# Performance work log

Measured on AMD Instinct MI355X. Metric: run time of the kernel, lower is better.

Reference implementation:

```python
import jax, jax.numpy as jnp
import numpy as np

B, N, D = 2, 2048, 1024
H = 16
HD = D // H
SCALE = HD ** -0.5


def setup_inputs() -> dict:
    key = jax.random.key(0)
    k1, k2, kw, kb = jax.random.split(key, 4)
    x1 = jax.random.normal(k1, (B, N, D), dtype=jnp.float32)
    x2 = jax.random.normal(k2, (B, N, D), dtype=jnp.float32)
    # fused qkv linear: torch nn.Linear(dim, 3*dim): W [3D, D], b [3D]
    bound = 1.0 / np.sqrt(D)
    qkv_w = jax.random.uniform(kw, (3 * D, D), minval=-bound, maxval=bound, dtype=jnp.float32)
    qkv_b = jax.random.uniform(kb, (3 * D,), minval=-bound, maxval=bound, dtype=jnp.float32)
    return {"x1": x1, "x2": x2, "qkv_w": qkv_w, "qkv_b": qkv_b}


def reference(x1, x2, qkv_w, qkv_b):
    # qkv projections (only q from x1 and k,v from x2 are used by the module)
    q1 = (jnp.einsum('bnd,ed->bne', x1, qkv_w[:D]) + qkv_b[:D])
    k2 = (jnp.einsum('bnd,ed->bne', x2, qkv_w[D:2 * D]) + qkv_b[D:2 * D])
    v2 = (jnp.einsum('bnd,ed->bne', x2, qkv_w[2 * D:]) + qkv_b[2 * D:])
    # [B, H, N, HD]
    q1 = q1.reshape(B, N, H, HD).transpose(0, 2, 1, 3)
    k2 = k2.reshape(B, N, H, HD).transpose(0, 2, 1, 3)
    v2 = v2.reshape(B, N, H, HD).transpose(0, 2, 1, 3)
    # explicit QK^T -> softmax -> AV (materializes [B,H,N,N] like the original)
    scores = jnp.einsum('bhqd,bhkd->bhqk', q1, k2) * SCALE
    attn = jax.nn.softmax(scores, axis=-1)
    out = jnp.einsum('bhqk,bhkd->bhqd', attn, v2)
    # [B, N, D]; note original module skips out_proj (never applied in forward)
    return out.transpose(0, 2, 1, 3).reshape(B, N, D)
```

## Files before the change

kernel.cpp:

```cpp
#include <hip/hip_runtime.h>
#include <cstdint>
#include <cstddef>

#define B_   2
#define N_   2048
#define D_   1024
#define H_   16
#define HD_  64
#define QSCALE_ 0.18033688011112042f

typedef unsigned short u16;
typedef unsigned int   u32;
typedef __attribute__((ext_vector_type(8))) short short8;
typedef __attribute__((ext_vector_type(4))) float f32x4;
typedef __attribute__((ext_vector_type(4))) float fl4;
typedef __attribute__((ext_vector_type(4))) unsigned short us4;

__device__ __forceinline__ u16 f2bf(float f) {
  u32 u = __builtin_bit_cast(u32, f);
  u += 0x7fffu + ((u >> 16) & 1u);
  return (u16)(u >> 16);
}

__device__ __forceinline__ void gload16(const void* g, void* l) {
  typedef __attribute__((address_space(1))) unsigned int gu32;
  typedef __attribute__((address_space(3))) unsigned int lu32;
  __builtin_amdgcn_global_load_lds((gu32*)g, (lu32*)l, 16, 0, 0);
}

__global__ void convert_kernel(const fl4* __restrict__ x1, const fl4* __restrict__ x2,
                               const fl4* __restrict__ w,
                               us4* __restrict__ o1, us4* __restrict__ o2,
                               us4* __restrict__ ow) {
  const int NX = (B_ * N_ * D_) / 4;
  const int NW = (3 * D_ * D_) / 4;
  int stride = gridDim.x * blockDim.x;
  for (int i = blockIdx.x * blockDim.x + threadIdx.x; i < NX; i += stride) {
    fl4 a = x1[i];
    us4 r; r.x = f2bf(a.x); r.y = f2bf(a.y); r.z = f2bf(a.z); r.w = f2bf(a.w);
    o1[i] = r;
    fl4 b = x2[i];
    us4 s; s.x = f2bf(b.x); s.y = f2bf(b.y); s.z = f2bf(b.z); s.w = f2bf(b.w);
    o2[i] = s;
    if (i < NW) {
      fl4 c = w[i];
      us4 t; t.x = f2bf(c.x); t.y = f2bf(c.y); t.z = f2bf(c.z); t.w = f2bf(c.w);
      ow[i] = t;
    }
  }
}

__global__ __launch_bounds__(256) void qkv_gemm(
    const u16* __restrict__ x1b, const u16* __restrict__ x2b,
    const u16* __restrict__ wb, const float* __restrict__ bias,
    u16* __restrict__ Qb, u16* __restrict__ Kb, u16* __restrict__ Vtb) {
  const int z = blockIdx.z;
  const u16* X = (z == 0) ? x1b : x2b;
  const u16* W = wb + (size_t)z * D_ * D_;
  const float* bz = bias + z * D_;
  const int m0 = blockIdx.y * 128;
  const int e0 = blockIdx.x * 128;
  const int tid = threadIdx.x;
  const int lane = tid & 63;
  const int w = tid >> 6;
  const int wr = w >> 1, wc = w & 1;
  const int col = lane & 15, quad = lane >> 4;

  __shared__ __align__(16) u16 As[128 * 32];
  __shared__ __align__(16) u16 Bs[128 * 32];

  f32x4 acc[4][4] = {};

  int off0 = w * 2048 + lane * 16;
  int row0 = off0 >> 6;
  int ke0  = (off0 & 63) >> 1;
  int off1 = off0 + 1024;
  int row1 = off1 >> 6;
  int ke1  = (off1 & 63) >> 1;

  const u16* gA0 = X + (size_t)(m0 + row0) * D_ + ke0;
  const u16* gA1 = X + (size_t)(m0 + row1) * D_ + ke1;
  const u16* gB0 = W + (size_t)(e0 + row0) * D_ + ke0;
  const u16* gB1 = W + (size_t)(e0 + row1) * D_ + ke1;
  u16* lA0 = &As[w * 1024];
  u16* lA1 = &As[w * 1024 + 512];
  u16* lB0 = &Bs[w * 1024];
  u16* lB1 = &Bs[w * 1024 + 512];

  for (int k0 = 0; k0 < D_; k0 += 32) {
    __syncthreads();
    gload16(gA0 + k0, lA0);
    gload16(gA1 + k0, lA1);
    gload16(gB0 + k0, lB0);
    gload16(gB1 + k0, lB1);
    __syncthreads();

    short8 a[4], b[4];
#pragma unroll
    for (int i = 0; i < 4; ++i)
      a[i] = *(const short8*)&As[(wr * 64 + i * 16 + col) * 32 + quad * 8];
#pragma unroll
    for (int j = 0; j < 4; ++j)
      b[j] = *(const short8*)&Bs[(wc * 64 + j * 16 + col) * 32 + quad * 8];
#pragma unroll
    for (int i = 0; i < 4; ++i)
#pragma unroll
      for (int j = 0; j < 4; ++j)
        acc[i][j] = __builtin_amdgcn_mfma_f32_16x16x32_bf16(a[i], b[j], acc[i][j], 0, 0, 0);
  }

#pragma unroll
  for (int j = 0; j < 4; ++j) {
    int eg = e0 + wc * 64 + j * 16 + col;
    float bj = bz[eg];
    int h = eg >> 6, d = eg & 63;
#pragma unroll
    for (int i = 0; i < 4; ++i) {
#pragma unroll
      for (int r = 0; r < 4; ++r) {
        int m = m0 + wr * 64 + i * 16 + quad * 4 + r;
        int bb = m >> 11, n = m & (N_ - 1);
        float v = acc[i][j][r] + bj;
        if (z == 0) v *= QSCALE_;
        u16 o = f2bf(v);
        if (z == 0)      Qb [(((size_t)bb * H_ + h) * N_ + n) * HD_ + d] = o;
        else if (z == 1) Kb [(((size_t)bb * H_ + h) * N_ + n) * HD_ + d] = o;
        else             Vtb[(((size_t)bb * H_ + h) * HD_ + d) * N_ + n] = o;
      }
    }
  }
}

__global__ __launch_bounds__(256) void attn_kernel(
    const u16* __restrict__ Qb, const u16* __restrict__ Kb,
    const u16* __restrict__ Vtb, float* __restrict__ out) {
  const int bh = blockIdx.y;
  const int bb = bh >> 4, h = bh & 15;
  const int q0 = blockIdx.x * 64;
  const int tid = threadIdx.x;
  const int lane = tid & 63;
  const int w = tid >> 6;
  const int col = lane & 15, quad = lane >> 4;

  const u16* __restrict__ Q  = Qb  + ((size_t)bh << 17);
  const u16* __restrict__ K  = Kb  + ((size_t)bh << 17);
  const u16* __restrict__ Vt = Vtb + ((size_t)bh << 17);

  __shared__ __align__(16) u16 Ks[64 * 72];
  __shared__ __align__(16) u16 Vs[64 * 72];
  __shared__ __align__(16) u16 P[4][16 * 72];
  u16* Pw = P[w];

  const int qrow = q0 + w * 16 + col;
  short8 qa0 = *(const short8*)&Q[qrow * HD_ + quad * 8];
  short8 qa1 = *(const short8*)&Q[qrow * HD_ + 32 + quad * 8];

  const int srow = tid >> 3;
  const int sseg = (tid & 7) * 8;
  const u16* gK0 = &K[srow * HD_ + sseg];
  const u16* gK1 = &K[(srow + 32) * HD_ + sseg];
  const u16* gV0 = &Vt[srow * N_ + sseg];
  const u16* gV1 = &Vt[(srow + 32) * N_ + sseg];
  u16* lK0 = &Ks[srow * 72 + sseg];
  u16* lK1 = &Ks[(srow + 32) * 72 + sseg];
  u16* lV0 = &Vs[srow * 72 + sseg];
  u16* lV1 = &Vs[(srow + 32) * 72 + sseg];

  f32x4 accO[4] = {};
  float lsum[4] = {0.f, 0.f, 0.f, 0.f};

  short8 kA = *(const short8*)(gK0);
  short8 kB = *(const short8*)(gK1);
  short8 vA = *(const short8*)(gV0);
  short8 vB = *(const short8*)(gV1);

  for (int k0 = 0; k0 < N_; k0 += 64) {
    __syncthreads();
    *(short8*)lK0 = kA;
    *(short8*)lK1 = kB;
    *(short8*)lV0 = vA;
    *(short8*)lV1 = vB;
    if (k0 + 64 < N_) {
      kA = *(const short8*)(gK0 + (k0 + 64) * HD_);
      kB = *(const short8*)(gK1 + (k0 + 64) * HD_);
      vA = *(const short8*)(gV0 + (k0 + 64));
      vB = *(const short8*)(gV1 + (k0 + 64));
    }
    __syncthreads();

    f32x4 s[4] = {};
#pragma unroll
    for (int jn = 0; jn < 4; ++jn) {
      short8 kb0 = *(const short8*)&Ks[(jn * 16 + col) * 72 + quad * 8];
      short8 kb1 = *(const short8*)&Ks[(jn * 16 + col) * 72 + 32 + quad * 8];
      s[jn] = __builtin_amdgcn_mfma_f32_16x16x32_bf16(qa0, kb0, s[jn], 0, 0, 0);
      s[jn] = __builtin_amdgcn_mfma_f32_16x16x32_bf16(qa1, kb1, s[jn], 0, 0, 0);
    }

#pragma unroll
    for (int jn = 0; jn < 4; ++jn)
#pragma unroll
      for (int r = 0; r < 4; ++r) {
        float e = exp2f(s[jn][r]);
        lsum[r] += e;
        Pw[(quad * 4 + r) * 72 + jn * 16 + col] =
            (u16)(__builtin_bit_cast(u32, e) >> 16);
      }
    __asm__ volatile("" ::: "memory");
    short8 pa0 = *(const short8*)&Pw[col * 72 + quad * 8];
    short8 pa1 = *(const short8*)&Pw[col * 72 + 32 + quad * 8];
    __asm__ volatile("" ::: "memory");

#pragma unroll
    for (int jd = 0; jd < 4; ++jd) {
      short8 vb0 = *(const short8*)&Vs[(jd * 16 + col) * 72 + quad * 8];
      short8 vb1 = *(const short8*)&Vs[(jd * 16 + col) * 72 + 32 + quad * 8];
      accO[jd] = __builtin_amdgcn_mfma_f32_16x16x32_bf16(pa0, vb0, accO[jd], 0, 0, 0);
      accO[jd] = __builtin_amdgcn_mfma_f32_16x16x32_bf16(pa1, vb1, accO[jd], 0, 0, 0);
    }
  }

#pragma unroll
  for (int r = 0; r < 4; ++r) {
    float v = lsum[r];
    v += __shfl_xor(v, 1);
    v += __shfl_xor(v, 2);
    v += __shfl_xor(v, 4);
    v += __shfl_xor(v, 8);
    lsum[r] = 1.0f / v;
  }

#pragma unroll
  for (int jd = 0; jd < 4; ++jd)
#pragma unroll
    for (int r = 0; r < 4; ++r) {
      int n = q0 + w * 16 + quad * 4 + r;
      int e = h * HD_ + jd * 16 + col;
      out[((size_t)bb * N_ + n) * D_ + e] = accO[jd][r] * lsum[r];
    }
}

extern "C" void kernel_launch(void* const* d_in, const int* in_sizes, int n_in,
                              void* d_out, int out_size, void* d_ws, size_t ws_size,
                              hipStream_t stream) {
  const float* x1 = (const float*)d_in[0];
  const float* x2 = (const float*)d_in[1];
  const float* qw = (const float*)d_in[2];
  const float* qb = (const float*)d_in[3];
  float* out = (float*)d_out;

  u16* ws   = (u16*)d_ws;
  u16* x1b  = ws;
  u16* x2b  = ws + 4194304;
  u16* wb   = ws + 8388608;
  u16* Qbf  = ws + 11534336;
  u16* Kbf  = ws + 15728640;
  u16* Vtb  = ws + 19922944;
  if (ws_size < (size_t)24117248 * 2) return;

  convert_kernel<<<dim3(1024), dim3(256), 0, stream>>>(
      (const fl4*)x1, (const fl4*)x2, (const fl4*)qw,
      (us4*)x1b, (us4*)x2b, (us4*)wb);

  qkv_gemm<<<dim3(8, 32, 3), dim3(256), 0, stream>>>(
      x1b, x2b, wb, qb, Qbf, Kbf, Vtb);

  attn_kernel<<<dim3(32, 32), dim3(256), 0, stream>>>(Qbf, Kbf, Vtb, out);
}
```

Baseline: 205.0 us.

## Double-buffer K/V tiles in attention with XOR-swizzled LDS and one barrier

```diff
diff --git a/kernel.cpp b/kernel.cpp
--- a/kernel.cpp
+++ b/kernel.cpp
@@ -15,6 +15,12 @@
 typedef __attribute__((ext_vector_type(4))) float f32x4;
 typedef __attribute__((ext_vector_type(4))) float fl4;
 typedef __attribute__((ext_vector_type(4))) unsigned short us4;
+
+#if __has_builtin(__builtin_amdgcn_exp2f)
+#define EXP2F(x) __builtin_amdgcn_exp2f(x)
+#else
+#define EXP2F(x) exp2f(x)
+#endif
 
 __device__ __forceinline__ u16 f2bf(float f) {
   u32 u = __builtin_bit_cast(u32, f);
@@ -131,7 +137,7 @@
   }
 }
 
-__global__ __launch_bounds__(256) void attn_kernel(
+__global__ __launch_bounds__(256, 4) void attn_kernel(
     const u16* __restrict__ Qb, const u16* __restrict__ Kb,
     const u16* __restrict__ Vtb, float* __restrict__ out) {
   const int bh = blockIdx.y;
@@ -146,77 +152,98 @@
   const u16* __restrict__ K  = Kb  + ((size_t)bh << 17);
   const u16* __restrict__ Vt = Vtb + ((size_t)bh << 17);
 
-  __shared__ __align__(16) u16 Ks[64 * 72];
-  __shared__ __align__(16) u16 Vs[64 * 72];
-  __shared__ __align__(16) u16 P[4][16 * 72];
+  __shared__ __align__(16) u16 Ks[2][64 * 64];
+  __shared__ __align__(16) u16 Vs[2][64 * 64];
+  __shared__ __align__(16) u16 P[4][16 * 64];
   u16* Pw = P[w];
 
   const int qrow = q0 + w * 16 + col;
   short8 qa0 = *(const short8*)&Q[qrow * HD_ + quad * 8];
   short8 qa1 = *(const short8*)&Q[qrow * HD_ + 32 + quad * 8];
 
+  const int g0  = (quad ^ (col & 7)) * 8;
+  const int g4  = g0 ^ 32;
+  const int pg0 = (quad ^ ((col >> 1) & 7)) * 8;
+  const int pg4 = pg0 ^ 32;
+  const int c3 = col >> 3, c7 = col & 7;
+  const int h2 = quad * 2;
+
   const int srow = tid >> 3;
-  const int sseg = (tid & 7) * 8;
-  const u16* gK0 = &K[srow * HD_ + sseg];
-  const u16* gK1 = &K[(srow + 32) * HD_ + sseg];
-  const u16* gV0 = &Vt[srow * N_ + sseg];
-  const u16* gV1 = &Vt[(srow + 32) * N_ + sseg];
-  u16* lK0 = &Ks[srow * 72 + sseg];
-  u16* lK1 = &Ks[(srow + 32) * 72 + sseg];
-  u16* lV0 = &Vs[srow * 72 + sseg];
-  u16* lV1 = &Vs[(srow + 32) * 72 + sseg];
+  const int sg   = tid & 7;
+  const int lw0 = srow * 64 + ((sg ^ (srow & 7)) * 8);
+  const int lw1 = lw0 + 2048;
+  const u16* gK = K + tid * 8;
+  const u16* gV = Vt + srow * N_ + sg * 8;
 
   f32x4 accO[4] = {};
   float lsum[4] = {0.f, 0.f, 0.f, 0.f};
 
-  short8 kA = *(const short8*)(gK0);
-  short8 kB = *(const short8*)(gK1);
-  short8 vA = *(const short8*)(gV0);
-  short8 vB = *(const short8*)(gV1);
-
-  for (int k0 = 0; k0 < N_; k0 += 64) {
+  short8 kA = *(const short8*)(gK);
+  short8 kB = *(const short8*)(gK + 2048);
+  short8 vA = *(const short8*)(gV);
+  short8 vB = *(const short8*)(gV + 32 * N_);
+  *(short8*)&Ks[0][lw0] = kA;
+  *(short8*)&Ks[0][lw1] = kB;
+  *(short8*)&Vs[0][lw0] = vA;
+  *(short8*)&Vs[0][lw1] = vB;
+
+  for (int t = 0; t < N_ / 64; ++t) {
     __syncthreads();
-    *(short8*)lK0 = kA;
-    *(short8*)lK1 = kB;
-    *(short8*)lV0 = vA;
-    *(short8*)lV1 = vB;
-    if (k0 + 64 < N_) {
-      kA = *(const short8*)(gK0 + (k0 + 64) * HD_);
-      kB = *(const short8*)(gK1 + (k0 + 64) * HD_);
-      vA = *(const short8*)(gV0 + (k0 + 64));
-      vB = *(const short8*)(gV1 + (k0 + 64));
-    }
-    __syncthreads();
+    const int cur = t & 1;
+    if (t < N_ / 64 - 1) {
+      const int k0n = (t + 1) * 64;
+      kA = *(const short8*)(gK + k0n * 64);
+      kB = *(const short8*)(gK + k0n * 64 + 2048);
+      vA = *(const short8*)(gV + k0n);
+      vB = *(const short8*)(gV + k0n + 32 * N_);
+    }
+    const u16* Kc = Ks[cur];
+    const u16* Vc = Vs[cur];
 
     f32x4 s[4] = {};
+    __builtin_amdgcn_s_setprio(1);
 #pragma unroll
     for (int jn = 0; jn < 4; ++jn) {
-      short8 kb0 = *(const short8*)&Ks[(jn * 16 + col) * 72 + quad * 8];
-      short8 kb1 = *(const short8*)&Ks[(jn * 16 + col) * 72 + 32 + quad * 8];
+      const int rb = (jn * 16 + col) * 64;
+      short8 kb0 = *(const short8*)&Kc[rb + g0];
+      short8 kb1 = *(const short8*)&Kc[rb + g4];
       s[jn] = __builtin_amdgcn_mfma_f32_16x16x32_bf16(qa0, kb0, s[jn], 0, 0, 0);
       s[jn] = __builtin_amdgcn_mfma_f32_16x16x32_bf16(qa1, kb1, s[jn], 0, 0, 0);
     }
+    __builtin_amdgcn_s_setprio(0);
 
 #pragma unroll
     for (int jn = 0; jn < 4; ++jn)
 #pragma unroll
       for (int r = 0; r < 4; ++r) {
-        float e = exp2f(s[jn][r]);
+        float e = EXP2F(s[jn][r]);
         lsum[r] += e;
-        Pw[(quad * 4 + r) * 72 + jn * 16 + col] =
+        Pw[(quad * 4 + r) * 64 + (((2 * jn + c3) ^ (h2 + (r >> 1))) * 8) + c7] =
             (u16)(__builtin_bit_cast(u32, e) >> 16);
       }
     __asm__ volatile("" ::: "memory");
-    short8 pa0 = *(const short8*)&Pw[col * 72 + quad * 8];
-    short8 pa1 = *(const short8*)&Pw[col * 72 + 32 + quad * 8];
+    short8 pa0 = *(const short8*)&Pw[col * 64 + pg0];
+    short8 pa1 = *(const short8*)&Pw[col * 64 + pg4];
     __asm__ volatile("" ::: "memory");
 
+    __builtin_amdgcn_s_setprio(1);
 #pragma unroll
     for (int jd = 0; jd < 4; ++jd) {
-      short8 vb0 = *(const short8*)&Vs[(jd * 16 + col) * 72 + quad * 8];
-      short8 vb1 = *(const short8*)&Vs[(jd * 16 + col) * 72 + 32 + quad * 8];
+      const int rb = (jd * 16 + col) * 64;
+      short8 vb0 = *(const short8*)&Vc[rb + g0];
+      short8 vb1 = *(const short8*)&Vc[rb + g4];
       accO[jd] = __builtin_amdgcn_mfma_f32_16x16x32_bf16(pa0, vb0, accO[jd], 0, 0, 0);
       accO[jd] = __builtin_amdgcn_mfma_f32_16x16x32_bf16(pa1, vb1, accO[jd], 0, 0, 0);
+    }
+    __builtin_amdgcn_s_setprio(0);
+
+    if (t < N_ / 64 - 1) {
+      u16* Kn = (u16*)Ks[cur ^ 1];
+      u16* Vn = (u16*)Vs[cur ^ 1];
+      *(short8*)&Kn[lw0] = kA;
+      *(short8*)&Kn[lw1] = kB;
+      *(short8*)&Vn[lw0] = vA;
+      *(short8*)&Vn[lw1] = vB;
     }
   }
 
```

After: 188.5 us. -8.1%, faster.
